# Performance work log

Measured on AMD Instinct MI355X. Metric: run time of the kernel, lower is better.

The kernel has to match this reference:

```python
import jax, jax.numpy as jnp
import numpy as np

N_NODES = 50000
N_RAND_EDGES = 800000  # plus N_NODES self-loop edges appended in setup
IN_FEATS, N_HIDDEN, N_CLASSES = 128, 64, 64


def setup_inputs() -> dict:
    key = jax.random.key(0)
    kf, ks, kd, k1, k2, k3 = jax.random.split(key, 6)
    features = jax.random.normal(kf, (N_NODES, IN_FEATS), dtype=jnp.float32)
    src = jax.random.randint(ks, (N_RAND_EDGES,), 0, N_NODES, dtype=jnp.int32)
    dst = jax.random.randint(kd, (N_RAND_EDGES,), 0, N_NODES, dtype=jnp.int32)
    # dgl.add_self_loop: append (i, i) for every node
    loop = jnp.arange(N_NODES, dtype=jnp.int32)
    src = jnp.concatenate([src, loop])
    dst = jnp.concatenate([dst, loop])

    def glorot(k, fan_in, fan_out):
        lim = jnp.sqrt(6.0 / (fan_in + fan_out)).astype(jnp.float32)
        return jax.random.uniform(k, (fan_in, fan_out), jnp.float32, -lim, lim)

    return {
        "features": features, "src": src, "dst": dst,
        "W1": glorot(k1, IN_FEATS, N_HIDDEN), "b1": jnp.zeros((N_HIDDEN,), jnp.float32),
        "W2": glorot(k2, N_HIDDEN, N_HIDDEN), "b2": jnp.zeros((N_HIDDEN,), jnp.float32),
        "W3": glorot(k3, N_HIDDEN, N_CLASSES), "b3": jnp.zeros((N_CLASSES,), jnp.float32),
    }


def _graph_conv(x, W, b, src, dst, norm_src_e, norm_dst_n, n_nodes):
    """DGL GraphConv, norm='both': D_dst^{-1/2} A D_src^{-1/2} X W + b, then relu."""
    if W.shape[0] > W.shape[1]:  # mult by W first when it shrinks the feature dim
        x = x @ W
        m = x[src] * norm_src_e[:, None]                      # [E, out]
        h = jax.ops.segment_sum(m, dst, num_segments=n_nodes)  # [N, out]
        h = h * norm_dst_n[:, None]
    else:
        m = x[src] * norm_src_e[:, None]                      # [E, in]
        h = jax.ops.segment_sum(m, dst, num_segments=n_nodes)  # [N, in]
        h = (h * norm_dst_n[:, None]) @ W
    return jax.nn.relu(h + b)


def reference(features, src, dst, W1, b1, W2, b2, W3, b3):
    n = features.shape[0]
    ones = jnp.ones(src.shape[0], dtype=features.dtype)
    out_deg = jax.ops.segment_sum(ones, src, num_segments=n)
    in_deg = jax.ops.segment_sum(ones, dst, num_segments=n)
    norm_out = jnp.where(out_deg > 0, jax.lax.rsqrt(jnp.maximum(out_deg, 1.0)), 0.0)
    norm_in = jnp.where(in_deg > 0, jax.lax.rsqrt(jnp.maximum(in_deg, 1.0)), 0.0)
    norm_src_e = norm_out[src]  # per-edge source normalization

    h1 = _graph_conv(features, W1, b1, src, dst, norm_src_e, norm_in, n)
    h2 = _graph_conv(h1, W2, b2, src, dst, norm_src_e, norm_in, n)
    h3 = _graph_conv(h2, W3, b3, src, dst, norm_src_e, norm_in, n)
    # JumpingKnowledge mode='max': elementwise max over stacked layer outputs
    return jnp.max(jnp.stack([h1, h2, h3], axis=0), axis=0)
```

## Files before the change

kernel.cpp:

```cpp
#include <hip/hip_runtime.h>

typedef _Float16 h16;
typedef __attribute__((ext_vector_type(4))) _Float16 half4;
typedef __attribute__((ext_vector_type(8))) _Float16 half8;
typedef __attribute__((ext_vector_type(8))) float float8;

#define RANGES 8
#define PPR    64
#define HTHREADS 1024
#define BINS   6400
#define HALF   (BINS / 2)
#define HWORDS (BINS)
#define NSEG   100
#define NFILL  (RANGES * PPR)

__global__ __launch_bounds__(HTHREADS) void hist_kernel(const int* __restrict__ src,
                                                        const int* __restrict__ dst,
                                                        int* __restrict__ partial, int E) {
  __shared__ int h[HWORDS];
  const int r = blockIdx.x >> 6;
  const int c = blockIdx.x & 63;
  for (int i = threadIdx.x; i < HWORDS; i += HTHREADS) h[i] = 0;
  __syncthreads();
  const int lo = r * BINS;
  const int chunk = (E + PPR - 1) / PPR;
  const int e0 = c * chunk;
  const int e1 = min(E, e0 + chunk);
  for (int e = e0 + threadIdx.x; e < e1; e += HTHREADS) {
    int s = src[e] - lo;
    if ((unsigned)s < (unsigned)BINS) atomicAdd(&h[s >> 1], 1 << ((s & 1) * 16));
    int d = dst[e] - lo;
    if ((unsigned)d < (unsigned)BINS) atomicAdd(&h[HALF + (d >> 1)], 1 << ((d & 1) * 16));
  }
  __syncthreads();
  int* op = partial + (size_t)blockIdx.x * HWORDS;
  for (int i = threadIdx.x; i < HWORDS; i += HTHREADS) op[i] = h[i];
}

__global__ __launch_bounds__(256) void reduce_norm_scan1(
    int* __restrict__ partial, float* __restrict__ nout, float* __restrict__ nin,
    int* __restrict__ rowptr, int* __restrict__ bsums, int N) {
  __shared__ int s[256];
  const int j = blockIdx.x * 256 + threadIdx.x;
  const int r = j / HALF;
  const int w = j % HALF;
  int* base = partial + (size_t)(r * PPR) * HWORDS;
  int sumO = 0, runI = 0;
#pragma unroll 8
  for (int p = 0; p < PPR; ++p) {
    sumO += base[(size_t)p * HWORDS + w];
    int vI = base[(size_t)p * HWORDS + HALF + w];
    base[(size_t)p * HWORDS + HALF + w] = runI;
    runI += vI;
  }
  const int od0 = sumO & 0xFFFF, od1 = (sumO >> 16) & 0xFFFF;
  const int id0 = runI & 0xFFFF, id1 = (runI >> 16) & 0xFFFF;
  const int n0 = 2 * j, n1 = n0 + 1;
  if (n0 < N) {
    nout[n0] = od0 > 0 ? rsqrtf((float)od0) : 0.f;
    nin[n0]  = id0 > 0 ? rsqrtf((float)id0) : 0.f;
  }
  if (n1 < N) {
    nout[n1] = od1 > 0 ? rsqrtf((float)od1) : 0.f;
    nin[n1]  = id1 > 0 ? rsqrtf((float)id1) : 0.f;
  }
  const int local = id0 + id1;
  int v = local;
  s[threadIdx.x] = v;
  __syncthreads();
#pragma unroll
  for (int off = 1; off < 256; off <<= 1) {
    int tv = 0;
    if (threadIdx.x >= off) tv = s[threadIdx.x - off];
    __syncthreads();
    if (threadIdx.x >= off) s[threadIdx.x] += tv;
    __syncthreads();
  }
  const int excl = s[threadIdx.x] - v;
  if (n0 < N) rowptr[n0] = excl;
  if (n1 < N) rowptr[n1] = excl + id0;
  if (threadIdx.x == 255) bsums[blockIdx.x] = s[255];
}

__global__ __launch_bounds__(HTHREADS) void fill_gemm_kernel(
    const int* __restrict__ src, const int* __restrict__ dst,
    const int* __restrict__ rowptr, const int* __restrict__ bsums,
    const int* __restrict__ partial, int* __restrict__ rowptr_abs,
    unsigned short* __restrict__ csr,
    const float* __restrict__ feat, const float* __restrict__ W1,
    const float* __restrict__ nout, half4* __restrict__ bufAh,
    int N, int E) {
  __shared__ __align__(16) char smem[51200];
  const int tid = threadIdx.x;

  if (blockIdx.x < NFILL) {
    int* cur = (int*)smem;
    int* top = (int*)(smem + BINS * 4);
    const int r = blockIdx.x & 7;
    const int c = blockIdx.x >> 3;
    if (tid < 128) top[tid] = (tid < NSEG) ? bsums[tid] : 0;
    __syncthreads();
#pragma unroll
    for (int off = 1; off < 128; off <<= 1) {
      int v = 0;
      if (tid < 128 && tid >= off) v = top[tid - off];
      __syncthreads();
      if (tid < 128 && tid >= off) top[tid] += v;
      __syncthreads();
    }
    const int lo = r * BINS;
    const int* pf = partial + (size_t)(r * PPR + c) * HWORDS + HALF;
    for (int n = tid; n < BINS; n += HTHREADS) {
      int g = lo + n;
      int rp = 0;
      if (g < N) {
        int seg = g >> 9;
        rp = rowptr[g] + (seg ? top[seg - 1] : 0);
        if (c == 0) rowptr_abs[g] = rp;
      }
      int pw = pf[n >> 1];
      cur[n] = rp + ((pw >> ((n & 1) * 16)) & 0xFFFF);
    }
    if (blockIdx.x == 0 && tid == 0) rowptr_abs[N] = E;
    __syncthreads();
    const int chunk = (E + PPR - 1) / PPR;
    const int e0 = c * chunk;
    const int e1 = min(E, e0 + chunk);
    for (int e = e0 + tid; e < e1; e += HTHREADS) {
      int d = dst[e] - lo;
      if ((unsigned)d < (unsigned)BINS) {
        int pos = atomicAdd(&cur[d], 1);
        csr[pos] = (unsigned short)src[e];
      }
    }
  } else {
    float* sA = (float*)smem;
    float* sB = (float*)(smem + 128 * 68 * 4);
    const int tile = blockIdx.x - NFILL;
    const int row0 = tile << 7;
    const int ry = tid >> 4;
    const int tx = tid & 15;
    const int r0 = 2 * ry, r1 = r0 + 1;
    float4 acc0 = make_float4(0.f, 0.f, 0.f, 0.f);
    float4 acc1 = make_float4(0.f, 0.f, 0.f, 0.f);
#pragma unroll
    for (int kc = 0; kc < 2; ++kc) {
      __syncthreads();
      for (int i = tid * 4; i < 128 * 64; i += HTHREADS * 4) {
        int rr = i >> 6, cc = i & 63;
        int gr = row0 + rr;
        float4 v = make_float4(0.f, 0.f, 0.f, 0.f);
        if (gr < N) v = *reinterpret_cast<const float4*>(feat + (size_t)gr * 128 + kc * 64 + cc);
        *reinterpret_cast<float4*>(sA + rr * 68 + cc) = v;
      }
      {
        int i = tid * 4;
        int rr = i >> 6, cc = i & 63;
        *reinterpret_cast<float4*>(sB + rr * 64 + cc) =
            *reinterpret_cast<const float4*>(W1 + (size_t)(kc * 64 + rr) * 64 + cc);
      }
      __syncthreads();
#pragma unroll 8
      for (int k = 0; k < 64; ++k) {
        float a0 = sA[r0 * 68 + k], a1 = sA[r1 * 68 + k];
        float4 b = *reinterpret_cast<float4*>(sB + k * 64 + tx * 4);
        acc0.x += a0 * b.x; acc0.y += a0 * b.y; acc0.z += a0 * b.z; acc0.w += a0 * b.w;
        acc1.x += a1 * b.x; acc1.y += a1 * b.y; acc1.z += a1 * b.z; acc1.w += a1 * b.w;
      }
    }
#pragma unroll
    for (int rr = 0; rr < 2; ++rr) {
      const int gr = row0 + (rr ? r1 : r0);
      if (gr >= N) continue;
      float4 v = rr ? acc1 : acc0;
      float no = nout[gr];
      half4 hv;
      hv.x = (h16)(v.x * no); hv.y = (h16)(v.y * no);
      hv.z = (h16)(v.z * no); hv.w = (h16)(v.w * no);
      bufAh[(size_t)gr * 16 + tx] = hv;
    }
  }
}

__device__ __forceinline__ float8 gather_row(const int* __restrict__ rowptr,
                                             const unsigned short* __restrict__ csr,
                                             const half8* __restrict__ xv,
                                             int node, int lane) {
  const int b = rowptr[node], e = rowptr[node + 1];
  float8 a0 = 0.f, a1 = 0.f, a2 = 0.f, a3 = 0.f;
  int i = b;
  for (; i + 8 <= e; i += 8) {
    int s0 = csr[i + 0], s1 = csr[i + 1], s2 = csr[i + 2], s3 = csr[i + 3];
    int s4 = csr[i + 4], s5 = csr[i + 5], s6 = csr[i + 6], s7 = csr[i + 7];
    half8 v0 = xv[(size_t)s0 * 8 + lane];
    half8 v1 = xv[(size_t)s1 * 8 + lane];
    half8 v2 = xv[(size_t)s2 * 8 + lane];
    half8 v3 = xv[(size_t)s3 * 8 + lane];
    half8 v4 = xv[(size_t)s4 * 8 + lane];
    half8 v5 = xv[(size_t)s5 * 8 + lane];
    half8 v6 = xv[(size_t)s6 * 8 + lane];
    half8 v7 = xv[(size_t)s7 * 8 + lane];
#pragma unroll
    for (int j = 0; j < 8; ++j) {
      a0[j] += (float)v0[j]; a1[j] += (float)v1[j];
      a2[j] += (float)v2[j]; a3[j] += (float)v3[j];
      a0[j] += (float)v4[j]; a1[j] += (float)v5[j];
      a2[j] += (float)v6[j]; a3[j] += (float)v7[j];
    }
  }
  for (; i + 4 <= e; i += 4) {
    int s0 = csr[i + 0], s1 = csr[i + 1], s2 = csr[i + 2], s3 = csr[i + 3];
    half8 v0 = xv[(size_t)s0 * 8 + lane];
    half8 v1 = xv[(size_t)s1 * 8 + lane];
    half8 v2 = xv[(size_t)s2 * 8 + lane];
    half8 v3 = xv[(size_t)s3 * 8 + lane];
#pragma unroll
    for (int j = 0; j < 8; ++j) {
      a0[j] += (float)v0[j]; a1[j] += (float)v1[j];
      a2[j] += (float)v2[j]; a3[j] += (float)v3[j];
    }
  }
  for (; i < e; ++i) {
    int s = csr[i];
    half8 v = xv[(size_t)s * 8 + lane];
#pragma unroll
    for (int j = 0; j < 8; ++j) a0[j] += (float)v[j];
  }
#pragma unroll
  for (int j = 0; j < 8; ++j) a0[j] = (a0[j] + a1[j]) + (a2[j] + a3[j]);
  return a0;
}

__global__ __launch_bounds__(512) void agg1_kernel(
    const int* __restrict__ rowptr, const unsigned short* __restrict__ csr,
    const h16* __restrict__ x, const float* __restrict__ nin,
    const float* __restrict__ bias, const float* __restrict__ nout,
    half8* __restrict__ y, float* __restrict__ out, int N) {
  int t = blockIdx.x * 512 + threadIdx.x;
  int node = t >> 3;
  if (node >= N) return;
  int lane = t & 7;
  float8 acc = gather_row(rowptr, csr, reinterpret_cast<const half8*>(x), node, lane);
  const float s = nin[node];
  const float no = nout[node];
  float8 h;
  half8 hv;
#pragma unroll
  for (int j = 0; j < 8; ++j) {
    h[j] = fmaxf(acc[j] * s + bias[lane * 8 + j], 0.f);
    hv[j] = (h16)(h[j] * no);
  }
  size_t off = (size_t)node * 64 + lane * 8;
  *reinterpret_cast<float4*>(out + off)     = make_float4(h[0], h[1], h[2], h[3]);
  *reinterpret_cast<float4*>(out + off + 4) = make_float4(h[4], h[5], h[6], h[7]);
  y[(size_t)node * 8 + lane] = hv;
}

template <bool WRITEC>
__global__ __launch_bounds__(512) void fused_layer(
    const int* __restrict__ rowptr, const unsigned short* __restrict__ csr,
    const h16* __restrict__ x, const float* __restrict__ W,
    const float* __restrict__ nin, const float* __restrict__ bias,
    const float* __restrict__ nout,
    half4* __restrict__ C, float* __restrict__ out, int N) {
  __shared__ float sA[64][68];
  __shared__ float sB[64][64];
  const int t = threadIdx.x;
  const int row0 = blockIdx.x * 64;

  for (int i = t * 4; i < 64 * 64; i += 512 * 4)
    *reinterpret_cast<float4*>(&sB[0][0] + i) = *reinterpret_cast<const float4*>(W + i);

  {
    const int node = t >> 3, lane = t & 7;
    const int g = row0 + node;
    float8 acc = 0.f;
    float s = 0.f;
    if (g < N) {
      acc = gather_row(rowptr, csr, reinterpret_cast<const half8*>(x), g, lane);
      s = nin[g];
    }
    *reinterpret_cast<float4*>(&sA[node][lane * 8]) =
        make_float4(acc[0] * s, acc[1] * s, acc[2] * s, acc[3] * s);
    *reinterpret_cast<float4*>(&sA[node][lane * 8 + 4]) =
        make_float4(acc[4] * s, acc[5] * s, acc[6] * s, acc[7] * s);
  }
  __syncthreads();

  const int tx = t & 15;
  const int ry = t >> 4;
  const int r0 = 2 * ry, r1 = r0 + 1;
  float4 a0 = make_float4(0.f, 0.f, 0.f, 0.f);
  float4 a1 = make_float4(0.f, 0.f, 0.f, 0.f);
#pragma unroll 8
  for (int k = 0; k < 64; ++k) {
    float x0 = sA[r0][k], x1 = sA[r1][k];
    float4 b = *reinterpret_cast<float4*>(&sB[k][tx * 4]);
    a0.x += x0 * b.x; a0.y += x0 * b.y; a0.z += x0 * b.z; a0.w += x0 * b.w;
    a1.x += x1 * b.x; a1.y += x1 * b.y; a1.z += x1 * b.z; a1.w += x1 * b.w;
  }

  const float4 bb = *reinterpret_cast<const float4*>(bias + tx * 4);
#pragma unroll
  for (int rr = 0; rr < 2; ++rr) {
    const int gr = row0 + (rr ? r1 : r0);
    if (gr >= N) continue;
    float4 v = rr ? a1 : a0;
    v.x = fmaxf(v.x + bb.x, 0.f);
    v.y = fmaxf(v.y + bb.y, 0.f);
    v.z = fmaxf(v.z + bb.z, 0.f);
    v.w = fmaxf(v.w + bb.w, 0.f);
    size_t off = (size_t)gr * 64 + tx * 4;
    float4 o = *reinterpret_cast<float4*>(out + off);
    o.x = fmaxf(o.x, v.x);
    o.y = fmaxf(o.y, v.y);
    o.z = fmaxf(o.z, v.z);
    o.w = fmaxf(o.w, v.w);
    *reinterpret_cast<float4*>(out + off) = o;
    if (WRITEC) {
      float no = nout[gr];
      half4 hv;
      hv.x = (h16)(v.x * no); hv.y = (h16)(v.y * no);
      hv.z = (h16)(v.z * no); hv.w = (h16)(v.w * no);
      C[(size_t)gr * 16 + tx] = hv;
    }
  }
}

extern "C" void kernel_launch(void* const* d_in, const int* in_sizes, int n_in,
                              void* d_out, int out_size, void* d_ws, size_t ws_size,
                              hipStream_t stream) {
  const float* feat = (const float*)d_in[0];
  const int* src    = (const int*)d_in[1];
  const int* dst    = (const int*)d_in[2];
  const float* W1   = (const float*)d_in[3];
  const float* b1   = (const float*)d_in[4];
  const float* W2   = (const float*)d_in[5];
  const float* b2   = (const float*)d_in[6];
  const float* W3   = (const float*)d_in[7];
  const float* b3   = (const float*)d_in[8];
  float* out = (float*)d_out;

  const int N = in_sizes[0] / 128;
  const int E = in_sizes[1];

  char* p = (char*)d_ws;
  float* nout       = (float*)p;     p += (size_t)N * 4;
  float* nin        = (float*)p;     p += (size_t)N * 4;
  int*   rowptr     = (int*)p;       p += ((size_t)N + 8) * 4;
  int*   rowptr_abs = (int*)p;       p += ((size_t)N + 8) * 4;
  int*   bsums      = (int*)p;       p += 1024 * 4;
  unsigned short* csr = (unsigned short*)p;  p += (((size_t)E + 8) & ~7) * 2;
  p = (char*)(((uintptr_t)p + 15) & ~(uintptr_t)15);
  h16*   bufAh = (h16*)p;            p += (size_t)N * 64 * 2;
  h16*   bufBh = (h16*)p;            p += (size_t)N * 64 * 2;
  p = (char*)(((uintptr_t)p + 15) & ~(uintptr_t)15);
  int*   partial = (int*)p;          p += (size_t)RANGES * PPR * HWORDS * 4;

  const int ngemm = (N + 127) / 128;

  hist_kernel<<<NFILL, HTHREADS, 0, stream>>>(src, dst, partial, E);
  reduce_norm_scan1<<<NSEG, 256, 0, stream>>>(partial, nout, nin, rowptr, bsums, N);
  fill_gemm_kernel<<<NFILL + ngemm, HTHREADS, 0, stream>>>(
      src, dst, rowptr, bsums, partial, rowptr_abs, csr,
      feat, W1, nout, (half4*)bufAh, N, E);

  const int gemm_blocks = (N + 63) / 64;
  const int agg1_blocks = (int)(((size_t)N * 8 + 511) / 512);

  agg1_kernel<<<agg1_blocks, 512, 0, stream>>>(rowptr_abs, csr, bufAh, nin, b1, nout,
                                               (half8*)bufBh, out, N);
  fused_layer<true><<<gemm_blocks, 512, 0, stream>>>(rowptr_abs, csr, bufBh, W2, nin, b2, nout,
                                                     (half4*)bufAh, out, N);
  fused_layer<false><<<gemm_blocks, 512, 0, stream>>>(rowptr_abs, csr, bufAh, W3, nin, b3, nullptr,
                                                      nullptr, out, N);
}
```

Measured before the change: 150.0 us.

## Pre-bucket edges by node range before histogram and CSR fill

Adds a bucketing pass that partitions edges into 8 node-range buckets, storing dst packed with src and src-local ids separately. The histogram and CSR fill kernels then each read only their range's bucket instead of scanning all edges 8 times. This cuts the redundant global reads of src/dst, but adds an extra kernel, a memset, global atomics on bucket cursors, and scattered bucket writes.

```diff
diff --git a/kernel.cpp b/kernel.cpp
--- a/kernel.cpp
+++ b/kernel.cpp
@@ -13,24 +13,70 @@
 #define HWORDS (BINS)
 #define NSEG   100
 #define NFILL  (RANGES * PPR)
-
-__global__ __launch_bounds__(HTHREADS) void hist_kernel(const int* __restrict__ src,
-                                                        const int* __restrict__ dst,
-                                                        int* __restrict__ partial, int E) {
+#define NBUCK  512
+
+__global__ __launch_bounds__(HTHREADS) void bucket_kernel(
+    const int* __restrict__ src, const int* __restrict__ dst,
+    unsigned int* __restrict__ dbucket, unsigned short* __restrict__ sbucket,
+    int* __restrict__ gcur, int E) {
+  __shared__ int cnt[16];
+  __shared__ int basep[16];
+  const int tid = threadIdx.x;
+  const int chunk = (E + NBUCK - 1) / NBUCK;
+  const int e0 = blockIdx.x * chunk;
+  const int e1 = min(E, e0 + chunk);
+  for (int base = e0; base < e1; base += HTHREADS) {
+    const int e = base + tid;
+    const bool valid = e < e1;
+    if (tid < 16) cnt[tid] = 0;
+    __syncthreads();
+    int s = 0, d = 0, kd = 0, ks = 0, offd = 0, offs = 0;
+    if (valid) {
+      s = src[e]; d = dst[e];
+      kd = d / BINS;
+      ks = 8 + s / BINS;
+      offd = atomicAdd(&cnt[kd], 1);
+      offs = atomicAdd(&cnt[ks], 1);
+    }
+    __syncthreads();
+    if (tid < 16) basep[tid] = atomicAdd(&gcur[tid], cnt[tid]);
+    __syncthreads();
+    if (valid) {
+      const int dl = d - kd * BINS;
+      dbucket[(size_t)kd * E + basep[kd] + offd] = ((unsigned)dl << 16) | (unsigned)s;
+      const int sl = s - (ks - 8) * BINS;
+      sbucket[(size_t)(ks - 8) * E + basep[ks] + offs] = (unsigned short)sl;
+    }
+  }
+}
+
+__global__ __launch_bounds__(HTHREADS) void hist_kernel(
+    const unsigned int* __restrict__ dbucket, const unsigned short* __restrict__ sbucket,
+    const int* __restrict__ gcur, int* __restrict__ partial, int E) {
   __shared__ int h[HWORDS];
   const int r = blockIdx.x >> 6;
   const int c = blockIdx.x & 63;
   for (int i = threadIdx.x; i < HWORDS; i += HTHREADS) h[i] = 0;
   __syncthreads();
-  const int lo = r * BINS;
-  const int chunk = (E + PPR - 1) / PPR;
-  const int e0 = c * chunk;
-  const int e1 = min(E, e0 + chunk);
-  for (int e = e0 + threadIdx.x; e < e1; e += HTHREADS) {
-    int s = src[e] - lo;
-    if ((unsigned)s < (unsigned)BINS) atomicAdd(&h[s >> 1], 1 << ((s & 1) * 16));
-    int d = dst[e] - lo;
-    if ((unsigned)d < (unsigned)BINS) atomicAdd(&h[HALF + (d >> 1)], 1 << ((d & 1) * 16));
+  {
+    const int L = gcur[8 + r];
+    const int cs = (L + PPR - 1) / PPR;
+    const int i0 = c * cs, i1 = min(L, i0 + cs);
+    const unsigned short* sb = sbucket + (size_t)r * E;
+    for (int i = i0 + threadIdx.x; i < i1; i += HTHREADS) {
+      int sl = sb[i];
+      atomicAdd(&h[sl >> 1], 1 << ((sl & 1) * 16));
+    }
+  }
+  {
+    const int L = gcur[r];
+    const int cs = (L + PPR - 1) / PPR;
+    const int i0 = c * cs, i1 = min(L, i0 + cs);
+    const unsigned int* db = dbucket + (size_t)r * E;
+    for (int i = i0 + threadIdx.x; i < i1; i += HTHREADS) {
+      int dl = db[i] >> 16;
+      atomicAdd(&h[HALF + (dl >> 1)], 1 << ((dl & 1) * 16));
+    }
   }
   __syncthreads();
   int* op = partial + (size_t)blockIdx.x * HWORDS;
@@ -83,7 +129,7 @@
 }
 
 __global__ __launch_bounds__(HTHREADS) void fill_gemm_kernel(
-    const int* __restrict__ src, const int* __restrict__ dst,
+    const unsigned int* __restrict__ dbucket, const int* __restrict__ gcur,
     const int* __restrict__ rowptr, const int* __restrict__ bsums,
     const int* __restrict__ partial, int* __restrict__ rowptr_abs,
     unsigned short* __restrict__ csr,
@@ -123,15 +169,14 @@
     }
     if (blockIdx.x == 0 && tid == 0) rowptr_abs[N] = E;
     __syncthreads();
-    const int chunk = (E + PPR - 1) / PPR;
-    const int e0 = c * chunk;
-    const int e1 = min(E, e0 + chunk);
-    for (int e = e0 + tid; e < e1; e += HTHREADS) {
-      int d = dst[e] - lo;
-      if ((unsigned)d < (unsigned)BINS) {
-        int pos = atomicAdd(&cur[d], 1);
-        csr[pos] = (unsigned short)src[e];
-      }
+    const int L = gcur[r];
+    const int cs = (L + PPR - 1) / PPR;
+    const int i0 = c * cs, i1 = min(L, i0 + cs);
+    const unsigned int* db = dbucket + (size_t)r * E;
+    for (int i = i0 + tid; i < i1; i += HTHREADS) {
+      unsigned int w = db[i];
+      int pos = atomicAdd(&cur[w >> 16], 1);
+      csr[pos] = (unsigned short)(w & 0xFFFF);
     }
   } else {
     float* sA = (float*)smem;
@@ -350,19 +395,25 @@
   int*   rowptr     = (int*)p;       p += ((size_t)N + 8) * 4;
   int*   rowptr_abs = (int*)p;       p += ((size_t)N + 8) * 4;
   int*   bsums      = (int*)p;       p += 1024 * 4;
+  int*   gcur       = (int*)p;       p += 64 * 4;
   unsigned short* csr = (unsigned short*)p;  p += (((size_t)E + 8) & ~7) * 2;
   p = (char*)(((uintptr_t)p + 15) & ~(uintptr_t)15);
   h16*   bufAh = (h16*)p;            p += (size_t)N * 64 * 2;
   h16*   bufBh = (h16*)p;            p += (size_t)N * 64 * 2;
   p = (char*)(((uintptr_t)p + 15) & ~(uintptr_t)15);
   int*   partial = (int*)p;          p += (size_t)RANGES * PPR * HWORDS * 4;
+  p = (char*)(((uintptr_t)p + 15) & ~(uintptr_t)15);
+  unsigned int* dbucket = (unsigned int*)p;  p += (size_t)RANGES * E * 4;
+  unsigned short* sbucket = (unsigned short*)p; p += (size_t)RANGES * E * 2;
 
   const int ngemm = (N + 127) / 128;
 
-  hist_kernel<<<NFILL, HTHREADS, 0, stream>>>(src, dst, partial, E);
+  hipMemsetAsync(gcur, 0, 16 * sizeof(int), stream);
+  bucket_kernel<<<NBUCK, HTHREADS, 0, stream>>>(src, dst, dbucket, sbucket, gcur, E);
+  hist_kernel<<<NFILL, HTHREADS, 0, stream>>>(dbucket, sbucket, gcur, partial, E);
   reduce_norm_scan1<<<NSEG, 256, 0, stream>>>(partial, nout, nin, rowptr, bsums, N);
   fill_gemm_kernel<<<NFILL + ngemm, HTHREADS, 0, stream>>>(
-      src, dst, rowptr, bsums, partial, rowptr_abs, csr,
+      dbucket, gcur, rowptr, bsums, partial, rowptr_abs, csr,
       feat, W1, nout, (half4*)bufAh, N, E);
 
   const int gemm_blocks = (N + 63) / 64;
```

New measurement: 158.3 us. 5.6% more time.
